# Performance work log

Measured on AMD Instinct MI355X. Metric: run time of the kernel, lower is better.

## Reference

```python
import jax, jax.numpy as jnp
import numpy as np


def setup_inputs() -> dict:
    key = jax.random.key(0)
    k1, k2 = jax.random.split(key)
    in_features, out_features, tokens = 4096, 4096, 8192
    x = jax.random.normal(k1, (tokens, in_features), dtype=jnp.float32)
    bound = 1.0 / np.sqrt(in_features)  # nn.Linear default init -> |W| <= 1
    W = jax.random.uniform(k2, (out_features, in_features), dtype=jnp.float32,
                           minval=-bound, maxval=bound)
    return {"x": x, "W": W}


def reference(x, W):
    # Forward of BinarizedLinear: y = x @ sign(W)^T (bias-free linear with
    # sign-binarized weights; the clamp_(-1,1) after sign() is a no-op).
    Wb = jnp.sign(W)  # [out, in], values in {-1, 0, +1}
    return jnp.einsum('ti,oi->to', x, Wb)  # [tokens, out]
```

## Files before the change

kernel.cpp:

```cpp
#include <hip/hip_runtime.h>
#include <hip/hip_bf16.h>
#include <stdint.h>

#define M_TOK 8192
#define N_OUT 4096
#define K_IN  4096

#define BM 256
#define BN 128
#define BKB 64
#define NT (K_IN / BKB)

typedef __attribute__((ext_vector_type(4))) int i32x4;

#define AS1 __attribute__((address_space(1)))
#define AS3 __attribute__((address_space(3)))
#define GLOAD_LDS16(g, l) \
  __builtin_amdgcn_global_load_lds((AS1 void*)(g), (AS3 void*)(l), 16, 0, 0)

#define BAR()     __builtin_amdgcn_s_barrier()
#define WAITALL() asm volatile("s_waitcnt vmcnt(0) lgkmcnt(0)" ::: "memory")
#define VMCNT6()  asm volatile("s_waitcnt vmcnt(6)" ::: "memory")
#define PRIO(p)   __builtin_amdgcn_s_setprio(p)
#define MFMAI8(a, b, c) __builtin_amdgcn_mfma_i32_16x16x64_i8((a), (b), (c), 0, 0, 0)

__global__ __launch_bounds__(256) void quant_x_i8(const float4* __restrict__ x,
                                                  int4* __restrict__ o,
                                                  float* __restrict__ scales) {
  const int row = blockIdx.x;
  const int t   = threadIdx.x;
  const float4* xr = x + (size_t)row * (K_IN / 4);
  float4 v[4];
  #pragma unroll
  for (int i = 0; i < 4; ++i) v[i] = xr[t * 4 + i];
  float m = 0.f;
  #pragma unroll
  for (int i = 0; i < 4; ++i)
    m = fmaxf(m, fmaxf(fmaxf(fabsf(v[i].x), fabsf(v[i].y)),
                       fmaxf(fabsf(v[i].z), fabsf(v[i].w))));
  #pragma unroll
  for (int off = 32; off; off >>= 1) m = fmaxf(m, __shfl_down(m, off));
  __shared__ float sm[4];
  if ((t & 63) == 0) sm[t >> 6] = m;
  __syncthreads();
  m = fmaxf(fmaxf(sm[0], sm[1]), fmaxf(sm[2], sm[3]));
  const float inv = m > 0.f ? 127.f / m : 0.f;
  if (t == 0) scales[row] = m > 0.f ? m / 127.f : 1.f;
  int q[4];
  #pragma unroll
  for (int i = 0; i < 4; ++i) {
    const int a0 = (int)rintf(v[i].x * inv);
    const int a1 = (int)rintf(v[i].y * inv);
    const int a2 = (int)rintf(v[i].z * inv);
    const int a3 = (int)rintf(v[i].w * inv);
    q[i] = (a0 & 255) | ((a1 & 255) << 8) | ((a2 & 255) << 16) | (a3 << 24);
  }
  o[(size_t)row * (K_IN / 16) + t] = make_int4(q[0], q[1], q[2], q[3]);
}

__global__ __launch_bounds__(256) void sgn_w_i8(const float4* __restrict__ w,
                                                int4* __restrict__ o, int n16) {
  int i = blockIdx.x * blockDim.x + threadIdx.x;
  int stride = gridDim.x * blockDim.x;
  for (; i < n16; i += stride) {
    int q[4];
    #pragma unroll
    for (int j = 0; j < 4; ++j) {
      float4 v = w[i * 4 + j];
      const int a0 = v.x > 0.f ? 1 : (v.x < 0.f ? -1 : 0);
      const int a1 = v.y > 0.f ? 1 : (v.y < 0.f ? -1 : 0);
      const int a2 = v.z > 0.f ? 1 : (v.z < 0.f ? -1 : 0);
      const int a3 = v.w > 0.f ? 1 : (v.w < 0.f ? -1 : 0);
      q[j] = (a0 & 255) | ((a1 & 255) << 8) | ((a2 & 255) << 16) | (a3 << 24);
    }
    o[i] = make_int4(q[0], q[1], q[2], q[3]);
  }
}

__global__ __launch_bounds__(256, 2) void bin_gemm_i8(const char* __restrict__ A,
                                                      const char* __restrict__ B,
                                                      const float* __restrict__ scales,
                                                      float* __restrict__ C) {
  __shared__ char lds[49152];

  const int tid  = threadIdx.x;
  const int w    = tid >> 6;
  const int lane = tid & 63;
  const int lr   = lane & 15;
  const int lk   = lane >> 4;
  const int wr   = w >> 1;
  const int wc   = w & 1;

  const int bm = blockIdx.x >> 5;
  const int bn = blockIdx.x & 31;

  const char* Ag = A + (size_t)bm * BM * K_IN;
  const char* Bg = B + (size_t)bn * BN * K_IN;

  const int ca0 = w * 256 + lane;
  const int cb0 = w * 128 + lane;
  size_t gA[4], gB[2];
  #pragma unroll
  for (int j = 0; j < 4; ++j) {
    const int c = ca0 + j * 64;
    const int r = c >> 2;
    gA[j] = (size_t)r * K_IN + (size_t)((((c & 3) ^ ((r >> 1) & 3))) << 4);
  }
  #pragma unroll
  for (int j = 0; j < 2; ++j) {
    const int c = cb0 + j * 64;
    const int r = c >> 2;
    gB[j] = (size_t)r * K_IN + (size_t)((((c & 3) ^ ((r >> 1) & 3))) << 4);
  }

  auto stage = [&](int tt) {
    const size_t koff = (size_t)tt * BKB;
    char* base = &lds[(tt & 1) * 24576];
    #pragma unroll
    for (int j = 0; j < 4; ++j)
      GLOAD_LDS16(Ag + gA[j] + koff, base + w * 4096 + j * 1024);
    #pragma unroll
    for (int j = 0; j < 2; ++j)
      GLOAD_LDS16(Bg + gB[j] + koff, base + 16384 + w * 2048 + j * 1024);
  };

  const int kof   = (lk ^ ((lr >> 1) & 3)) << 4;
  const int a_row = (wr * 128 + lr) * 64;
  const int b_row = 16384 + (wc * 64 + lr) * 64;

  i32x4 acc[8][4];
  #pragma unroll
  for (int m = 0; m < 8; ++m)
    #pragma unroll
    for (int n = 0; n < 4; ++n) { i32x4 z = {0, 0, 0, 0}; acc[m][n] = z; }

  stage(0);
  stage(1);
  VMCNT6();
  BAR();

  for (int t = 0; t < NT; ++t) {
    const char* L = &lds[(t & 1) * 24576];
    i32x4 aF[8], bF[4];

    #pragma unroll
    for (int m = 0; m < 8; ++m)
      aF[m] = *(const i32x4*)(L + a_row + m * 1024 + kof);
    #pragma unroll
    for (int n = 0; n < 4; ++n)
      bF[n] = *(const i32x4*)(L + b_row + n * 1024 + kof);
    PRIO(1);
    #pragma unroll
    for (int m = 0; m < 4; ++m)
      #pragma unroll
      for (int n = 0; n < 4; ++n)
        acc[m][n] = MFMAI8(aF[m], bF[n], acc[m][n]);
    PRIO(0);

    WAITALL();
    BAR();

    if (t + 2 < NT) stage(t + 2);
    PRIO(1);
    #pragma unroll
    for (int m = 4; m < 8; ++m)
      #pragma unroll
      for (int n = 0; n < 4; ++n)
        acc[m][n] = MFMAI8(aF[m], bF[n], acc[m][n]);
    PRIO(0);
  }

  const int grow0 = bm * BM + wr * 128;
  float scl[8][4];
  #pragma unroll
  for (int m = 0; m < 8; ++m)
    #pragma unroll
    for (int j = 0; j < 4; ++j)
      scl[m][j] = scales[grow0 + m * 16 + lk * 4 + j];

  float* Cp = C + (size_t)grow0 * N_OUT + bn * BN + wc * 64;
  #pragma unroll
  for (int m = 0; m < 8; ++m)
    #pragma unroll
    for (int n = 0; n < 4; ++n)
      #pragma unroll
      for (int j = 0; j < 4; ++j)
        Cp[(size_t)(m * 16 + lk * 4 + j) * N_OUT + n * 16 + lr] =
            (float)acc[m][n][j] * scl[m][j];
}

__global__ __launch_bounds__(256) void fb_gemm(const float* __restrict__ x,
                                               const float* __restrict__ W,
                                               float* __restrict__ y) {
  __shared__ float xs[32][33];
  __shared__ float ws[32][33];
  const int bx = blockIdx.x;
  const int by = blockIdx.y;
  const int tx = threadIdx.x & 31;
  const int ty = threadIdx.x >> 5;
  float acc[4] = {0.f, 0.f, 0.f, 0.f};
  for (int k0 = 0; k0 < K_IN; k0 += 32) {
    #pragma unroll
    for (int i = 0; i < 4; ++i) {
      int r = ty + i * 8;
      xs[r][tx] = x[(size_t)(by * 32 + r) * K_IN + k0 + tx];
      float wv = W[(size_t)(bx * 32 + r) * K_IN + k0 + tx];
      ws[r][tx] = wv > 0.f ? 1.f : (wv < 0.f ? -1.f : 0.f);
    }
    __syncthreads();
    #pragma unroll
    for (int i = 0; i < 4; ++i) {
      int r = ty + i * 8;
      float s = acc[i];
      #pragma unroll
      for (int k = 0; k < 32; ++k) s += xs[r][k] * ws[tx][k];
      acc[i] = s;
    }
    __syncthreads();
  }
  #pragma unroll
  for (int i = 0; i < 4; ++i)
    y[(size_t)(by * 32 + ty + i * 8) * N_OUT + bx * 32 + tx] = acc[i];
}

extern "C" void kernel_launch(void* const* d_in, const int* in_sizes, int n_in,
                              void* d_out, int out_size, void* d_ws, size_t ws_size,
                              hipStream_t stream) {
  const float* x = (const float*)d_in[0];
  const float* W = (const float*)d_in[1];
  float* y = (float*)d_out;

  const size_t need = (size_t)M_TOK * K_IN + (size_t)N_OUT * K_IN
                    + (size_t)M_TOK * sizeof(float);
  if (ws_size >= need) {
    char*  xq = (char*)d_ws;
    char*  wq = xq + (size_t)M_TOK * K_IN;
    float* sc = (float*)(wq + (size_t)N_OUT * K_IN);
    quant_x_i8<<<M_TOK, 256, 0, stream>>>((const float4*)x, (int4*)xq, sc);
    sgn_w_i8<<<2048, 256, 0, stream>>>((const float4*)W, (int4*)wq,
                                       N_OUT * K_IN / 16);
    bin_gemm_i8<<<(M_TOK / BM) * (N_OUT / BN), 256, 0, stream>>>(xq, wq, sc, y);
  } else {
    dim3 g(N_OUT / 32, M_TOK / 32);
    fb_gemm<<<g, 256, 0, stream>>>(x, W, y);
  }
}
```

Baseline: 196.2 us.

## Enlarge int8 GEMM tile to 256x256 with 512 threads and triple-buffered LDS

Doubles the output tile of the int8 GEMM from 256x128 to 256x256. It uses 8 waves per block arranged 2x4, so each loaded A and B byte is reused across more MFMAs and less global and LDS traffic is needed per output. LDS staging moves from double to triple buffering. The prefetch two tiles ahead is now issued at the start of each iteration, and vmcnt-based partial waits replace the full waitcnt, leaving one barrier per K-step. In exchange, LDS use grows to 96 KB per block, which limits occupancy to about one block per CU, and the grid shrinks to 512 blocks.

After: 188.6 us. -3.8%, faster.

```diff
diff --git a/kernel.cpp b/kernel.cpp
--- a/kernel.cpp
+++ b/kernel.cpp
@@ -7,7 +7,7 @@
 #define K_IN  4096
 
 #define BM 256
-#define BN 128
+#define BN 256
 #define BKB 64
 #define NT (K_IN / BKB)
 
@@ -19,8 +19,8 @@
   __builtin_amdgcn_global_load_lds((AS1 void*)(g), (AS3 void*)(l), 16, 0, 0)
 
 #define BAR()     __builtin_amdgcn_s_barrier()
-#define WAITALL() asm volatile("s_waitcnt vmcnt(0) lgkmcnt(0)" ::: "memory")
-#define VMCNT6()  asm volatile("s_waitcnt vmcnt(6)" ::: "memory")
+#define VMCNT4()  asm volatile("s_waitcnt vmcnt(4)" ::: "memory")
+#define VMCNT0()  asm volatile("s_waitcnt vmcnt(0)" ::: "memory")
 #define PRIO(p)   __builtin_amdgcn_s_setprio(p)
 #define MFMAI8(a, b, c) __builtin_amdgcn_mfma_i32_16x16x64_i8((a), (b), (c), 0, 0, 0)
 
@@ -77,51 +77,42 @@
   }
 }
 
-__global__ __launch_bounds__(256, 2) void bin_gemm_i8(const char* __restrict__ A,
+__global__ __launch_bounds__(512, 2) void bin_gemm_i8(const char* __restrict__ A,
                                                       const char* __restrict__ B,
                                                       const float* __restrict__ scales,
                                                       float* __restrict__ C) {
-  __shared__ char lds[49152];
+  __shared__ char lds[98304];
 
   const int tid  = threadIdx.x;
   const int w    = tid >> 6;
   const int lane = tid & 63;
   const int lr   = lane & 15;
   const int lk   = lane >> 4;
-  const int wr   = w >> 1;
-  const int wc   = w & 1;
-
-  const int bm = blockIdx.x >> 5;
-  const int bn = blockIdx.x & 31;
+  const int wr   = w >> 2;
+  const int wc   = w & 3;
+
+  const int bm = blockIdx.x >> 4;
+  const int bn = blockIdx.x & 15;
 
   const char* Ag = A + (size_t)bm * BM * K_IN;
   const char* Bg = B + (size_t)bn * BN * K_IN;
 
-  const int ca0 = w * 256 + lane;
-  const int cb0 = w * 128 + lane;
-  size_t gA[4], gB[2];
-  #pragma unroll
-  for (int j = 0; j < 4; ++j) {
-    const int c = ca0 + j * 64;
-    const int r = c >> 2;
-    gA[j] = (size_t)r * K_IN + (size_t)((((c & 3) ^ ((r >> 1) & 3))) << 4);
-  }
-  #pragma unroll
-  for (int j = 0; j < 2; ++j) {
-    const int c = cb0 + j * 64;
-    const int r = c >> 2;
-    gB[j] = (size_t)r * K_IN + (size_t)((((c & 3) ^ ((r >> 1) & 3))) << 4);
-  }
-
-  auto stage = [&](int tt) {
+  const int c0 = w * 128 + lane;
+  const int c1 = c0 + 64;
+  const int ra0 = c0 >> 2, ra1 = c1 >> 2;
+  const size_t g0 = (size_t)ra0 * K_IN
+                  + (size_t)((((c0 & 3) ^ ((ra0 >> 1) & 3))) << 4);
+  const size_t g1 = (size_t)ra1 * K_IN
+                  + (size_t)((((c1 & 3) ^ ((ra1 >> 1) & 3))) << 4);
+  const int ldsw = w * 2048;
+
+  auto stage = [&](int tt, int bufoff) {
     const size_t koff = (size_t)tt * BKB;
-    char* base = &lds[(tt & 1) * 24576];
-    #pragma unroll
-    for (int j = 0; j < 4; ++j)
-      GLOAD_LDS16(Ag + gA[j] + koff, base + w * 4096 + j * 1024);
-    #pragma unroll
-    for (int j = 0; j < 2; ++j)
-      GLOAD_LDS16(Bg + gB[j] + koff, base + 16384 + w * 2048 + j * 1024);
+    char* base = &lds[bufoff];
+    GLOAD_LDS16(Ag + g0 + koff, base + ldsw);
+    GLOAD_LDS16(Ag + g1 + koff, base + ldsw + 1024);
+    GLOAD_LDS16(Bg + g0 + koff, base + 16384 + ldsw);
+    GLOAD_LDS16(Bg + g1 + koff, base + 16384 + ldsw + 1024);
   };
 
   const int kof   = (lk ^ ((lr >> 1) & 3)) << 4;
@@ -134,40 +125,37 @@
     #pragma unroll
     for (int n = 0; n < 4; ++n) { i32x4 z = {0, 0, 0, 0}; acc[m][n] = z; }
 
-  stage(0);
-  stage(1);
-  VMCNT6();
+  stage(0, 0);
+  stage(1, 32768);
+  VMCNT4();
   BAR();
 
+  int oc = 0, on = 32768, op = 65536;
   for (int t = 0; t < NT; ++t) {
-    const char* L = &lds[(t & 1) * 24576];
+    const char* L = &lds[oc];
+
+    if (t + 2 < NT) stage(t + 2, op);
+
     i32x4 aF[8], bF[4];
-
     #pragma unroll
     for (int m = 0; m < 8; ++m)
       aF[m] = *(const i32x4*)(L + a_row + m * 1024 + kof);
     #pragma unroll
     for (int n = 0; n < 4; ++n)
       bF[n] = *(const i32x4*)(L + b_row + n * 1024 + kof);
+
     PRIO(1);
     #pragma unroll
-    for (int m = 0; m < 4; ++m)
+    for (int m = 0; m < 8; ++m)
       #pragma unroll
       for (int n = 0; n < 4; ++n)
         acc[m][n] = MFMAI8(aF[m], bF[n], acc[m][n]);
     PRIO(0);
 
-    WAITALL();
+    if (t < NT - 2) { VMCNT4(); } else { VMCNT0(); }
     BAR();
 
-    if (t + 2 < NT) stage(t + 2);
-    PRIO(1);
-    #pragma unroll
-    for (int m = 4; m < 8; ++m)
-      #pragma unroll
-      for (int n = 0; n < 4; ++n)
-        acc[m][n] = MFMAI8(aF[m], bF[n], acc[m][n]);
-    PRIO(0);
+    const int tmp = oc; oc = on; on = op; op = tmp;
   }
 
   const int grow0 = bm * BM + wr * 128;
@@ -239,7 +227,7 @@
     quant_x_i8<<<M_TOK, 256, 0, stream>>>((const float4*)x, (int4*)xq, sc);
     sgn_w_i8<<<2048, 256, 0, stream>>>((const float4*)W, (int4*)wq,
                                        N_OUT * K_IN / 16);
-    bin_gemm_i8<<<(M_TOK / BM) * (N_OUT / BN), 256, 0, stream>>>(xq, wq, sc, y);
+    bin_gemm_i8<<<(M_TOK / BM) * (N_OUT / BN), 512, 0, stream>>>(xq, wq, sc, y);
   } else {
     dim3 g(N_OUT / 32, M_TOK / 32);
     fb_gemm<<<g, 256, 0, stream>>>(x, W, y);
```
